# Kernel tuning notes

Measured on AMD Instinct MI355X. Metric: run time of the kernel, lower is better.

## Reference

```python
import jax, jax.numpy as jnp
import numpy as np

N, D = 8192, 1024  # tokens, model dim (d == D required by residual add)


def setup_inputs() -> dict:
    key = jax.random.key(0)
    ks = jax.random.split(key, 6)
    s = 1.0 / np.sqrt(D)
    return {
        "x": jax.random.normal(ks[0], (N, D), dtype=jnp.float32),
        "Wq": jax.random.normal(ks[1], (D, D), dtype=jnp.float32) * s,
        "Wk": jax.random.normal(ks[2], (D, D), dtype=jnp.float32) * s,
        "Wg": jax.random.normal(ks[3], (D, D), dtype=jnp.float32) * s,
        "Wm_w": jax.random.normal(ks[4], (D, 1), dtype=jnp.float32) * s,
        "Wm_b": jnp.zeros((1,), dtype=jnp.float32),
        "c": jnp.asarray(1.0 / np.sqrt(D), dtype=jnp.float32),
    }


def reference(x, Wq, Wk, Wg, Wm_w, Wm_b, c):
    # projections [N, d]
    q_hat = x @ Wq
    k_hat = x @ Wk
    # mean-center over the token axis
    q = q_hat - jnp.mean(q_hat, axis=0, keepdims=True)
    k = k_hat - jnp.mean(k_hat, axis=0, keepdims=True)
    # scaled scores [N, N], row softmax
    attn = jax.nn.softmax(c * (q @ k.T), axis=-1)
    # per-token gate m [N, 1], softmax over tokens, broadcast over columns
    m = x @ Wm_w + Wm_b
    gate = jax.nn.softmax(m, axis=0)
    omega = attn + gate  # [N, N]
    g = x @ Wg           # [N, d]
    return omega @ g + x  # residual, requires d == D
```

## Files before the change

### kernel.cpp

```cpp
#include <hip/hip_runtime.h>
#include <math.h>


#define NT 8192
#define DD 1024

typedef float v4f __attribute__((ext_vector_type(4)));
typedef short v8s __attribute__((ext_vector_type(8)));
typedef int   v4i __attribute__((ext_vector_type(4)));
typedef int   v8i __attribute__((ext_vector_type(8)));

typedef const __attribute__((address_space(1))) void* gp_t;
typedef __attribute__((address_space(3))) void* lp_t;

__device__ __forceinline__ short f2b(float f) {
    unsigned u = __float_as_uint(f);
    return (short)((u + 0x7fffu + ((u >> 16) & 1u)) >> 16);
}
__device__ __forceinline__ float b2f(short s) {
    return __uint_as_float(((unsigned)(unsigned short)s) << 16);
}
__device__ __forceinline__ char f2e4m3(float f) {
    unsigned p = __builtin_amdgcn_cvt_pk_fp8_f32(f, f, 0, false);
    return (char)(p & 0xff);
}

__device__ __forceinline__ void tile_coords(int bid, int tn, int& bm, int& bn) {
    const int SUP = 16;
    int per = SUP * tn;
    int band = bid / per, r = bid % per;
    bm = band * SUP + (r % SUP);
    bn = r / SUP;
}

__device__ __forceinline__ void gemm_core(const short* __restrict__ A,
                                          const short* __restrict__ B,
                                          int K, int m0, int n0,
                                          short* smem, v4f (&acc)[4][4])
{
    short* lsA = smem;
    short* lsB = smem + 8192;
    const int tid  = threadIdx.x;
    const int wave = tid >> 6, lane = tid & 63;
    const int l15 = lane & 15, l4 = lane >> 4;
    const int wm = (wave >> 1) << 6, wn = (wave & 1) << 6;

#pragma unroll
    for (int i = 0; i < 4; i++)
#pragma unroll
        for (int j = 0; j < 4; j++) acc[i][j] = (v4f)(0.0f);

    const int srow = lane >> 3;
    const int g    = (lane & 7) ^ srow;

    for (int k0 = 0; k0 < K; k0 += 64) {
#pragma unroll
        for (int i = 0; i < 4; i++) {
            int ci  = wave * 4 + i;
            int row = ci * 8 + srow;
            const short* ga = A + (size_t)(m0 + row) * K + k0 + g * 8;
            const short* gb = B + (size_t)(n0 + row) * K + k0 + g * 8;
            __builtin_amdgcn_global_load_lds((gp_t)ga, (lp_t)(lsA + ci * 512), 16, 0, 0);
            __builtin_amdgcn_global_load_lds((gp_t)gb, (lp_t)(lsB + ci * 512), 16, 0, 0);
        }
        __syncthreads();
#pragma unroll
        for (int kk = 0; kk < 64; kk += 32) {
            v8s af[4], bf[4];
#pragma unroll
            for (int t = 0; t < 4; t++) {
                int ra = wm + t * 16 + l15;
                int ca = ((kk >> 3) + l4) ^ (ra & 7);
                af[t] = *(const v8s*)(lsA + ra * 64 + ca * 8);
                int rb = wn + t * 16 + l15;
                int cb = ((kk >> 3) + l4) ^ (rb & 7);
                bf[t] = *(const v8s*)(lsB + rb * 64 + cb * 8);
            }
#pragma unroll
            for (int i = 0; i < 4; i++)
#pragma unroll
                for (int j = 0; j < 4; j++)
                    acc[i][j] = __builtin_amdgcn_mfma_f32_16x16x32_bf16(af[i], bf[j], acc[i][j], 0, 0, 0);
        }
        __syncthreads();
    }
}

__device__ __forceinline__ void gemm_core_mx(const char* __restrict__ A,
                                             const char* __restrict__ B,
                                             int K, int m0, int n0,
                                             char* smem, v4f (&acc)[4][4])
{
    char* lsA = smem;
    char* lsB = smem + 16384;
    const int tid  = threadIdx.x;
    const int wave = tid >> 6, lane = tid & 63;
    const int l15 = lane & 15, l4 = lane >> 4;
    const int wm = (wave >> 1) << 6, wn = (wave & 1) << 6;

#pragma unroll
    for (int i = 0; i < 4; i++)
#pragma unroll
        for (int j = 0; j < 4; j++) acc[i][j] = (v4f)(0.0f);

    const int srow = lane >> 3;
    const int g    = (lane & 7) ^ srow;

    for (int k0 = 0; k0 < K; k0 += 128) {
#pragma unroll
        for (int i = 0; i < 4; i++) {
            int ci  = wave * 4 + i;
            int row = ci * 8 + srow;
            const char* ga = A + (size_t)(m0 + row) * K + k0 + g * 16;
            const char* gb = B + (size_t)(n0 + row) * K + k0 + g * 16;
            __builtin_amdgcn_global_load_lds((gp_t)ga, (lp_t)(lsA + ci * 1024), 16, 0, 0);
            __builtin_amdgcn_global_load_lds((gp_t)gb, (lp_t)(lsB + ci * 1024), 16, 0, 0);
        }
        __syncthreads();
        v8i af[4], bq[4];
#pragma unroll
        for (int t = 0; t < 4; t++) {
            int ra = wm + t * 16 + l15;
            int a0 = (2 * l4) ^ (ra & 7), a1 = (2 * l4 + 1) ^ (ra & 7);
            v4i lo = *(const v4i*)(lsA + ra * 128 + a0 * 16);
            v4i hi = *(const v4i*)(lsA + ra * 128 + a1 * 16);
            af[t][0] = lo[0]; af[t][1] = lo[1]; af[t][2] = lo[2]; af[t][3] = lo[3];
            af[t][4] = hi[0]; af[t][5] = hi[1]; af[t][6] = hi[2]; af[t][7] = hi[3];
            int rb = wn + t * 16 + l15;
            int b0 = (2 * l4) ^ (rb & 7), b1 = (2 * l4 + 1) ^ (rb & 7);
            v4i blo = *(const v4i*)(lsB + rb * 128 + b0 * 16);
            v4i bhi = *(const v4i*)(lsB + rb * 128 + b1 * 16);
            bq[t][0] = blo[0]; bq[t][1] = blo[1]; bq[t][2] = blo[2]; bq[t][3] = blo[3];
            bq[t][4] = bhi[0]; bq[t][5] = bhi[1]; bq[t][6] = bhi[2]; bq[t][7] = bhi[3];
        }
#pragma unroll
        for (int i = 0; i < 4; i++)
#pragma unroll
            for (int j = 0; j < 4; j++)
                acc[i][j] = __builtin_amdgcn_mfma_scale_f32_16x16x128_f8f6f4(
                    af[i], bq[j], acc[i][j], 0, 0,
                    0, 0x7f7f7f7f, 0, 0x7f7f7f7f);
        __syncthreads();
    }
}


__global__ void cvt_x(const float* __restrict__ x, short* __restrict__ xb) {
    size_t i = ((size_t)blockIdx.x * 256 + threadIdx.x) * 8;
    float4 a = *(const float4*)(x + i);
    float4 b = *(const float4*)(x + i + 4);
    v8s o;
    o[0] = f2b(a.x); o[1] = f2b(a.y); o[2] = f2b(a.z); o[3] = f2b(a.w);
    o[4] = f2b(b.x); o[5] = f2b(b.y); o[6] = f2b(b.z); o[7] = f2b(b.w);
    *(v8s*)(xb + i) = o;
}

__global__ void cvt_w(const float* __restrict__ Wq, const float* __restrict__ Wk,
                      const float* __restrict__ Wg, short* __restrict__ wbt) {
    __shared__ float t[64][68];
    const float* W = blockIdx.z == 0 ? Wq : (blockIdx.z == 1 ? Wk : Wg);
    int k0 = blockIdx.x * 64, n0 = blockIdx.y * 64;
    int tr = threadIdx.x >> 4, tc = threadIdx.x & 15;
#pragma unroll
    for (int p = 0; p < 4; p++) {
        int r = p * 16 + tr;
        float4 v = *(const float4*)(W + (size_t)(k0 + r) * DD + n0 + tc * 4);
        t[r][tc * 4 + 0] = v.x; t[r][tc * 4 + 1] = v.y;
        t[r][tc * 4 + 2] = v.z; t[r][tc * 4 + 3] = v.w;
    }
    __syncthreads();
#pragma unroll
    for (int p = 0; p < 4; p++) {
        int rr = p * 16 + tr;
        short4 s;
        s.x = f2b(t[tc * 4 + 0][rr]); s.y = f2b(t[tc * 4 + 1][rr]);
        s.z = f2b(t[tc * 4 + 2][rr]); s.w = f2b(t[tc * 4 + 3][rr]);
        *(short4*)(wbt + (size_t)(blockIdx.z * DD + n0 + rr) * DD + k0 + tc * 4) = s;
    }
}

__global__ void gemv_m(const float* __restrict__ x, const float* __restrict__ wv,
                       const float* __restrict__ bp, float* __restrict__ mout) {
    int row = blockIdx.x * 4 + (threadIdx.x >> 6);
    int lane = threadIdx.x & 63;
    const float* xr = x + (size_t)row * DD;
    float s = 0.f;
    for (int c = lane * 4; c < DD; c += 256) {
        float4 a = *(const float4*)(xr + c);
        float4 b = *(const float4*)(wv + c);
        s = fmaf(a.x, b.x, s); s = fmaf(a.y, b.y, s);
        s = fmaf(a.z, b.z, s); s = fmaf(a.w, b.w, s);
    }
    for (int o = 32; o; o >>= 1) s += __shfl_down(s, o);
    if (lane == 0) mout[row] = s + bp[0];
}

__global__ void gate_k(const float* __restrict__ m, float* __restrict__ gate) {
    __shared__ float sred[4];
    __shared__ float sbc[2];
    int tid = threadIdx.x, lane = tid & 63, wave = tid >> 6;
    float mx = -3.4e38f;
    for (int i = tid; i < NT; i += 256) mx = fmaxf(mx, m[i]);
    for (int o = 32; o; o >>= 1) mx = fmaxf(mx, __shfl_xor(mx, o));
    if (lane == 0) sred[wave] = mx;
    __syncthreads();
    if (tid == 0) sbc[0] = fmaxf(fmaxf(sred[0], sred[1]), fmaxf(sred[2], sred[3]));
    __syncthreads();
    float gmax = sbc[0];
    float s = 0.f;
    for (int i = tid; i < NT; i += 256) s += expf(m[i] - gmax);
    for (int o = 32; o; o >>= 1) s += __shfl_xor(s, o);
    if (lane == 0) sred[wave] = s;
    __syncthreads();
    if (tid == 0) sbc[1] = sred[0] + sred[1] + sred[2] + sred[3];
    __syncthreads();
    float inv = 1.f / sbc[1];
    for (int i = tid; i < NT; i += 256) gate[i] = expf(m[i] - gmax) * inv;
}

__global__ void beta_gemv(const char* __restrict__ k8, const float* __restrict__ qsum,
                          const float* __restrict__ cp, float* __restrict__ beta) {
    int row = blockIdx.x * 4 + (threadIdx.x >> 6);
    int lane = threadIdx.x & 63;
    v4i kv = *(const v4i*)(k8 + (size_t)row * DD + lane * 16);
    const float* qs = qsum + lane * 16;
    float s = 0.f;
#pragma unroll
    for (int w = 0; w < 4; w++) {
        float4 qv = *(const float4*)(qs + w * 4);
        int word = kv[w];
        s = fmaf(__builtin_amdgcn_cvt_f32_fp8(word, 0), qv.x, s);
        s = fmaf(__builtin_amdgcn_cvt_f32_fp8(word, 1), qv.y, s);
        s = fmaf(__builtin_amdgcn_cvt_f32_fp8(word, 2), qv.z, s);
        s = fmaf(__builtin_amdgcn_cvt_f32_fp8(word, 3), qv.w, s);
    }
    for (int o = 32; o; o >>= 1) s += __shfl_down(s, o);
    if (lane == 0) beta[row] = s * cp[0] / (float)NT;
}


__global__ __launch_bounds__(256, 2) void k_proj(
        const short* __restrict__ xb, const short* __restrict__ wbt,
        char* __restrict__ q8, char* __restrict__ k8, char* __restrict__ gbt,
        float* __restrict__ qsum, float* __restrict__ gsum) {
    __shared__ __align__(16) short smem[16384];
    int bm, bn; tile_coords(blockIdx.x, 24, bm, bn);
    int m0 = bm * 128, n0 = bn * 128;
    v4f acc[4][4];
    gemm_core(xb, wbt, DD, m0, n0, smem, acc);

    const int tid = threadIdx.x, wave = tid >> 6, lane = tid & 63;
    const int l15 = lane & 15, l4 = lane >> 4;
    const int wm = (wave >> 1) << 6, wn = (wave & 1) << 6;
    int sec = n0 >> 10;
    int nloc = n0 & (DD - 1);

    if (sec < 2) {
        char* dst = sec ? k8 : q8;
        float cs[4] = {0.f, 0.f, 0.f, 0.f};
#pragma unroll
        for (int i = 0; i < 4; i++)
#pragma unroll
            for (int j = 0; j < 4; j++)
#pragma unroll
                for (int v = 0; v < 4; v++) {
                    int row = m0 + wm + i * 16 + l4 * 4 + v;
                    int col = nloc + wn + j * 16 + l15;
                    dst[(size_t)row * DD + col] = f2e4m3(acc[i][j][v]);
                    cs[j] += acc[i][j][v];
                }
        if (sec == 0)
#pragma unroll
            for (int j = 0; j < 4; j++)
                atomicAdd(&qsum[nloc + wn + j * 16 + l15], cs[j]);
    } else {
        char* sc = (char*)smem;
        float cs[4] = {0.f, 0.f, 0.f, 0.f};
#pragma unroll
        for (int i = 0; i < 4; i++)
#pragma unroll
            for (int j = 0; j < 4; j++)
#pragma unroll
                for (int v = 0; v < 4; v++) {
                    int lr = wn + j * 16 + l15;
                    int lc = wm + i * 16 + l4 * 4 + v;
                    sc[lr * 144 + lc] = f2e4m3(acc[i][j][v]);
                    cs[j] += acc[i][j][v];
                }
        __syncthreads();
#pragma unroll
        for (int it = 0; it < 4; it++) {
            int c = it * 256 + tid;
            int dr = c >> 3, cm = (c & 7) * 16;
            int4 vv = *(const int4*)(sc + dr * 144 + cm);
            *(int4*)(gbt + (size_t)(nloc + dr) * NT + m0 + cm) = vv;
        }
#pragma unroll
        for (int j = 0; j < 4; j++)
            atomicAdd(&gsum[nloc + wn + j * 16 + l15], cs[j]);
    }
}

__global__ __launch_bounds__(256, 2) void k_score(
        const char* __restrict__ q8, const char* __restrict__ k8,
        char* __restrict__ E, float* __restrict__ l, const float* __restrict__ cptr,
        const float* __restrict__ beta) {
    __shared__ __align__(16) char smem[32768];
    int bm, bn; tile_coords(blockIdx.x, 64, bm, bn);
    int m0 = bm * 128, n0 = bn * 128;
    v4f acc[4][4];
    gemm_core_mx(q8, k8, DD, m0, n0, smem, acc);

    const float cv = cptr[0];
    const int tid = threadIdx.x, wave = tid >> 6, lane = tid & 63;
    const int l15 = lane & 15, l4 = lane >> 4;
    const int wm = (wave >> 1) << 6, wn = (wave & 1) << 6;
    float bj[4];
#pragma unroll
    for (int j = 0; j < 4; j++) bj[j] = beta[n0 + wn + j * 16 + l15];
#pragma unroll
    for (int i = 0; i < 4; i++)
#pragma unroll
        for (int v = 0; v < 4; v++) {
            int row = m0 + wm + i * 16 + l4 * 4 + v;
            float rsum = 0.f;
#pragma unroll
            for (int j = 0; j < 4; j++) {
                float e = __expf(cv * acc[i][j][v] - bj[j]);
                E[(size_t)row * NT + (n0 + wn + j * 16 + l15)] = f2e4m3(e);
                rsum += e;
            }
#pragma unroll
            for (int o = 1; o < 16; o <<= 1) rsum += __shfl_xor(rsum, o);
            if (l15 == 0) atomicAdd(&l[row], rsum);
        }
}

__global__ __launch_bounds__(256, 2) void k_out(
        const char* __restrict__ E, const char* __restrict__ gbt,
        const float* __restrict__ l, const float* __restrict__ gate,
        const float* __restrict__ gsum, const float* __restrict__ x,
        float* __restrict__ out) {
    __shared__ __align__(16) char smem[32768];
    int bm, bn; tile_coords(blockIdx.x, 8, bm, bn);
    int m0 = bm * 128, n0 = bn * 128;
    v4f acc[4][4];
    gemm_core_mx(E, gbt, NT, m0, n0, smem, acc);

    const int tid = threadIdx.x, wave = tid >> 6, lane = tid & 63;
    const int l15 = lane & 15, l4 = lane >> 4;
    const int wm = (wave >> 1) << 6, wn = (wave & 1) << 6;
#pragma unroll
    for (int i = 0; i < 4; i++)
#pragma unroll
        for (int v = 0; v < 4; v++) {
            int row = m0 + wm + i * 16 + l4 * 4 + v;
            float inv = 1.f / l[row];
            float gv  = gate[row];
#pragma unroll
            for (int j = 0; j < 4; j++) {
                int col = n0 + wn + j * 16 + l15;
                out[(size_t)row * DD + col] =
                    acc[i][j][v] * inv + gv * gsum[col] + x[(size_t)row * DD + col];
            }
        }
}


extern "C" void kernel_launch(void* const* d_in, const int* in_sizes, int n_in,
                              void* d_out, int out_size, void* d_ws, size_t ws_size,
                              hipStream_t stream) {
    const float* x  = (const float*)d_in[0];
    const float* Wq = (const float*)d_in[1];
    const float* Wk = (const float*)d_in[2];
    const float* Wg = (const float*)d_in[3];
    const float* Wm = (const float*)d_in[4];
    const float* Wb = (const float*)d_in[5];
    const float* cp = (const float*)d_in[6];
    float* out = (float*)d_out;

    char* w = (char*)d_ws;
    size_t off = 0;
    auto alloc = [&](size_t bytes) -> void* {
        void* p = w + off;
        off += (bytes + 255) & ~(size_t)255;
        return p;
    };
    char*  q8    = (char*)alloc((size_t)NT * DD);
    char*  k8    = (char*)alloc((size_t)NT * DD);
    char*  gbt   = (char*)alloc((size_t)DD * NT);
    short* wbt   = (short*)alloc((size_t)3 * DD * DD * 2);
    short* xb    = (short*)alloc((size_t)NT * DD * 2);
    char*  E     = (char*)alloc((size_t)NT * NT);
    float* stats = (float*)alloc((2 * DD + 4 * NT) * 4);
    float* qsum = stats;
    float* gsum = stats + DD;
    float* lrow = stats + 2 * DD;
    float* mvec = lrow + NT;
    float* gate = mvec + NT;
    float* beta = gate + NT;
    if (off > ws_size) return;

    hipMemsetAsync(stats, 0, (size_t)(2 * DD + NT) * 4, stream);

    cvt_x<<<NT * DD / (256 * 8), 256, 0, stream>>>(x, xb);
    cvt_w<<<dim3(16, 16, 3), 256, 0, stream>>>(Wq, Wk, Wg, wbt);
    gemv_m<<<NT / 4, 256, 0, stream>>>(x, Wm, Wb, mvec);
    gate_k<<<1, 256, 0, stream>>>(mvec, gate);
    k_proj<<<64 * 24, 256, 0, stream>>>(xb, wbt, q8, k8, gbt, qsum, gsum);
    beta_gemv<<<NT / 4, 256, 0, stream>>>(k8, qsum, cp, beta);
    k_score<<<64 * 64, 256, 0, stream>>>(q8, k8, E, lrow, cp, beta);
    k_out<<<64 * 8, 256, 0, stream>>>(E, gbt, lrow, gate, gsum, x, out);
}
```

Before: 410.5 us.

## Fuse x conversion with gate GEMV and use plain fp8 MFMA for scores

Merges the bf16 conversion of x, the gate GEMV and the gate softmax into one kernel. It computes exp(m) per row and accumulates the denominator atomically, which removes two launches, a second read of x, and the serial single-block gate kernel. The normalization by the denominator moves into k_out's epilogue. The score GEMM switches from the scaled 16x16x128 f8f6f4 MFMA to a new fp8 core using 16x16x32 fp8 MFMA and 64-bit LDS fragment loads. The gate now skips max-subtraction, so exp can overflow if gate logits are large.

After: 406.6 us. Within noise of the previous version (-0.9%).

```diff
diff --git a/kernel.cpp b/kernel.cpp
--- a/kernel.cpp
+++ b/kernel.cpp
@@ -16,9 +16,6 @@
 __device__ __forceinline__ short f2b(float f) {
     unsigned u = __float_as_uint(f);
     return (short)((u + 0x7fffu + ((u >> 16) & 1u)) >> 16);
-}
-__device__ __forceinline__ float b2f(short s) {
-    return __uint_as_float(((unsigned)(unsigned short)s) << 16);
 }
 __device__ __forceinline__ char f2e4m3(float f) {
     unsigned p = __builtin_amdgcn_cvt_pk_fp8_f32(f, f, 0, false);
@@ -81,6 +78,61 @@
 #pragma unroll
                 for (int j = 0; j < 4; j++)
                     acc[i][j] = __builtin_amdgcn_mfma_f32_16x16x32_bf16(af[i], bf[j], acc[i][j], 0, 0, 0);
+        }
+        __syncthreads();
+    }
+}
+
+__device__ __forceinline__ void gemm_core_fp8(const char* __restrict__ A,
+                                              const char* __restrict__ B,
+                                              int K, int m0, int n0,
+                                              char* smem, v4f (&acc)[4][4])
+{
+    char* lsA = smem;
+    char* lsB = smem + 16384;
+    const int tid  = threadIdx.x;
+    const int wave = tid >> 6, lane = tid & 63;
+    const int l15 = lane & 15, l4 = lane >> 4;
+    const int wm = (wave >> 1) << 6, wn = (wave & 1) << 6;
+
+#pragma unroll
+    for (int i = 0; i < 4; i++)
+#pragma unroll
+        for (int j = 0; j < 4; j++) acc[i][j] = (v4f)(0.0f);
+
+    const int srow = lane >> 3;
+    const int g    = (lane & 7) ^ srow;
+
+    for (int k0 = 0; k0 < K; k0 += 128) {
+#pragma unroll
+        for (int i = 0; i < 4; i++) {
+            int ci  = wave * 4 + i;
+            int row = ci * 8 + srow;
+            const char* ga = A + (size_t)(m0 + row) * K + k0 + g * 16;
+            const char* gb = B + (size_t)(n0 + row) * K + k0 + g * 16;
+            __builtin_amdgcn_global_load_lds((gp_t)ga, (lp_t)(lsA + ci * 1024), 16, 0, 0);
+            __builtin_amdgcn_global_load_lds((gp_t)gb, (lp_t)(lsB + ci * 1024), 16, 0, 0);
+        }
+        __syncthreads();
+#pragma unroll
+        for (int kk = 0; kk < 128; kk += 32) {
+            long af[4], bq[4];
+            const int cbase = (kk >> 4) + (l4 >> 1);
+            const int half  = (l4 & 1) * 8;
+#pragma unroll
+            for (int t = 0; t < 4; t++) {
+                int ra = wm + t * 16 + l15;
+                int ca = cbase ^ (ra & 7);
+                af[t] = *(const long*)(lsA + ra * 128 + ca * 16 + half);
+                int rb = wn + t * 16 + l15;
+                int cb = cbase ^ (rb & 7);
+                bq[t] = *(const long*)(lsB + rb * 128 + cb * 16 + half);
+            }
+#pragma unroll
+            for (int i = 0; i < 4; i++)
+#pragma unroll
+                for (int j = 0; j < 4; j++)
+                    acc[i][j] = __builtin_amdgcn_mfma_f32_16x16x32_fp8_fp8(af[i], bq[j], acc[i][j], 0, 0, 0);
         }
         __syncthreads();
     }
@@ -145,14 +197,34 @@
 }
 
 
-__global__ void cvt_x(const float* __restrict__ x, short* __restrict__ xb) {
-    size_t i = ((size_t)blockIdx.x * 256 + threadIdx.x) * 8;
-    float4 a = *(const float4*)(x + i);
-    float4 b = *(const float4*)(x + i + 4);
-    v8s o;
-    o[0] = f2b(a.x); o[1] = f2b(a.y); o[2] = f2b(a.z); o[3] = f2b(a.w);
-    o[4] = f2b(b.x); o[5] = f2b(b.y); o[6] = f2b(b.z); o[7] = f2b(b.w);
-    *(v8s*)(xb + i) = o;
+__global__ void x_prep(const float* __restrict__ x, const float* __restrict__ wv,
+                       const float* __restrict__ bp, short* __restrict__ xb,
+                       float* __restrict__ em, float* __restrict__ gden) {
+    __shared__ float sred[4];
+    int wv_id = threadIdx.x >> 6;
+    int row = blockIdx.x * 4 + wv_id;
+    int lane = threadIdx.x & 63;
+    const float* xr = x + (size_t)row * DD;
+    short* xbr = xb + (size_t)row * DD;
+    float s = 0.f;
+    for (int c = lane * 4; c < DD; c += 256) {
+        float4 a = *(const float4*)(xr + c);
+        float4 b = *(const float4*)(wv + c);
+        s = fmaf(a.x, b.x, s); s = fmaf(a.y, b.y, s);
+        s = fmaf(a.z, b.z, s); s = fmaf(a.w, b.w, s);
+        short4 o;
+        o.x = f2b(a.x); o.y = f2b(a.y); o.z = f2b(a.z); o.w = f2b(a.w);
+        *(short4*)(xbr + c) = o;
+    }
+    for (int o = 32; o; o >>= 1) s += __shfl_down(s, o);
+    if (lane == 0) {
+        float e = __expf(s + bp[0]);
+        em[row] = e;
+        sred[wv_id] = e;
+    }
+    __syncthreads();
+    if (threadIdx.x == 0)
+        atomicAdd(gden, sred[0] + sred[1] + sred[2] + sred[3]);
 }
 
 __global__ void cvt_w(const float* __restrict__ Wq, const float* __restrict__ Wk,
@@ -177,45 +249,6 @@
         s.z = f2b(t[tc * 4 + 2][rr]); s.w = f2b(t[tc * 4 + 3][rr]);
         *(short4*)(wbt + (size_t)(blockIdx.z * DD + n0 + rr) * DD + k0 + tc * 4) = s;
     }
-}
-
-__global__ void gemv_m(const float* __restrict__ x, const float* __restrict__ wv,
-                       const float* __restrict__ bp, float* __restrict__ mout) {
-    int row = blockIdx.x * 4 + (threadIdx.x >> 6);
-    int lane = threadIdx.x & 63;
-    const float* xr = x + (size_t)row * DD;
-    float s = 0.f;
-    for (int c = lane * 4; c < DD; c += 256) {
-        float4 a = *(const float4*)(xr + c);
-        float4 b = *(const float4*)(wv + c);
-        s = fmaf(a.x, b.x, s); s = fmaf(a.y, b.y, s);
-        s = fmaf(a.z, b.z, s); s = fmaf(a.w, b.w, s);
-    }
-    for (int o = 32; o; o >>= 1) s += __shfl_down(s, o);
-    if (lane == 0) mout[row] = s + bp[0];
-}
-
-__global__ void gate_k(const float* __restrict__ m, float* __restrict__ gate) {
-    __shared__ float sred[4];
-    __shared__ float sbc[2];
-    int tid = threadIdx.x, lane = tid & 63, wave = tid >> 6;
-    float mx = -3.4e38f;
-    for (int i = tid; i < NT; i += 256) mx = fmaxf(mx, m[i]);
-    for (int o = 32; o; o >>= 1) mx = fmaxf(mx, __shfl_xor(mx, o));
-    if (lane == 0) sred[wave] = mx;
-    __syncthreads();
-    if (tid == 0) sbc[0] = fmaxf(fmaxf(sred[0], sred[1]), fmaxf(sred[2], sred[3]));
-    __syncthreads();
-    float gmax = sbc[0];
-    float s = 0.f;
-    for (int i = tid; i < NT; i += 256) s += expf(m[i] - gmax);
-    for (int o = 32; o; o >>= 1) s += __shfl_xor(s, o);
-    if (lane == 0) sred[wave] = s;
-    __syncthreads();
-    if (tid == 0) sbc[1] = sred[0] + sred[1] + sred[2] + sred[3];
-    __syncthreads();
-    float inv = 1.f / sbc[1];
-    for (int i = tid; i < NT; i += 256) gate[i] = expf(m[i] - gmax) * inv;
 }
 
 __global__ void beta_gemv(const char* __restrict__ k8, const float* __restrict__ qsum,
@@ -309,7 +342,7 @@
     int bm, bn; tile_coords(blockIdx.x, 64, bm, bn);
     int m0 = bm * 128, n0 = bn * 128;
     v4f acc[4][4];
-    gemm_core_mx(q8, k8, DD, m0, n0, smem, acc);
+    gemm_core_fp8(q8, k8, DD, m0, n0, smem, acc);
 
     const float cv = cptr[0];
     const int tid = threadIdx.x, wave = tid >> 6, lane = tid & 63;
@@ -338,15 +371,16 @@
 
 __global__ __launch_bounds__(256, 2) void k_out(
         const char* __restrict__ E, const char* __restrict__ gbt,
-        const float* __restrict__ l, const float* __restrict__ gate,
-        const float* __restrict__ gsum, const float* __restrict__ x,
-        float* __restrict__ out) {
+        const float* __restrict__ l, const float* __restrict__ em,
+        const float* __restrict__ gden, const float* __restrict__ gsum,
+        const float* __restrict__ x, float* __restrict__ out) {
     __shared__ __align__(16) char smem[32768];
     int bm, bn; tile_coords(blockIdx.x, 8, bm, bn);
     int m0 = bm * 128, n0 = bn * 128;
     v4f acc[4][4];
     gemm_core_mx(E, gbt, NT, m0, n0, smem, acc);
 
+    const float ginv = 1.f / gden[0];
     const int tid = threadIdx.x, wave = tid >> 6, lane = tid & 63;
     const int l15 = lane & 15, l4 = lane >> 4;
     const int wm = (wave >> 1) << 6, wn = (wave & 1) << 6;
@@ -356,7 +390,7 @@
         for (int v = 0; v < 4; v++) {
             int row = m0 + wm + i * 16 + l4 * 4 + v;
             float inv = 1.f / l[row];
-            float gv  = gate[row];
+            float gv  = em[row] * ginv;
 #pragma unroll
             for (int j = 0; j < 4; j++) {
                 int col = n0 + wn + j * 16 + l15;
@@ -392,23 +426,21 @@
     short* wbt   = (short*)alloc((size_t)3 * DD * DD * 2);
     short* xb    = (short*)alloc((size_t)NT * DD * 2);
     char*  E     = (char*)alloc((size_t)NT * NT);
-    float* stats = (float*)alloc((2 * DD + 4 * NT) * 4);
+    float* stats = (float*)alloc((2 * DD + 3 * NT + 1) * 4);
     float* qsum = stats;
     float* gsum = stats + DD;
     float* lrow = stats + 2 * DD;
-    float* mvec = lrow + NT;
-    float* gate = mvec + NT;
-    float* beta = gate + NT;
+    float* gden = lrow + NT;
+    float* em   = gden + 1;
+    float* beta = em + NT;
     if (off > ws_size) return;
 
-    hipMemsetAsync(stats, 0, (size_t)(2 * DD + NT) * 4, stream);
-
-    cvt_x<<<NT * DD / (256 * 8), 256, 0, stream>>>(x, xb);
+    hipMemsetAsync(stats, 0, (size_t)(2 * DD + NT + 1) * 4, stream);
+
+    x_prep<<<NT / 4, 256, 0, stream>>>(x, Wm, Wb, xb, em, gden);
     cvt_w<<<dim3(16, 16, 3), 256, 0, stream>>>(Wq, Wk, Wg, wbt);
-    gemv_m<<<NT / 4, 256, 0, stream>>>(x, Wm, Wb, mvec);
-    gate_k<<<1, 256, 0, stream>>>(mvec, gate);
     k_proj<<<64 * 24, 256, 0, stream>>>(xb, wbt, q8, k8, gbt, qsum, gsum);
     beta_gemv<<<NT / 4, 256, 0, stream>>>(k8, qsum, cp, beta);
     k_score<<<64 * 64, 256, 0, stream>>>(q8, k8, E, lrow, cp, beta);
-    k_out<<<64 * 8, 256, 0, stream>>>(E, gbt, lrow, gate, gsum, x, out);
-}
+    k_out<<<64 * 8, 256, 0, stream>>>(E, gbt, lrow, em, gden, gsum, x, out);
+}
```
